# Optimization experiments

Measured on AMD Instinct MI355X. Metric: run time of the kernel, lower is better.

The kernel has to match this reference:

```python
import jax, jax.numpy as jnp
import numpy as np

B, C, H, W = 2, 512, 128, 128
L_NUM, HEADS, LEVELS, POINTS = 6, 8, 1, 4
HEAD_DIM = C // HEADS


def setup_inputs() -> dict:
    key = jax.random.key(0)
    ks = jax.random.split(key, 16)
    s = 0.02
    rn = lambda k, shape, scale=s: jax.random.normal(k, shape, jnp.float32) * scale
    return dict(
        bev_feat=jax.random.normal(ks[0], (B, C, H, W), jnp.float32),
        lidar_feat=jax.random.normal(ks[1], (B, C, H, W), jnp.float32),
        Wv=rn(ks[2], (L_NUM, C, C)), bv=jnp.zeros((L_NUM, C), jnp.float32),
        Woff=rn(ks[3], (L_NUM, C, HEADS * LEVELS * POINTS * 2)),
        boff=rn(ks[4], (L_NUM, HEADS * LEVELS * POINTS * 2), 0.5),
        Waw=rn(ks[5], (L_NUM, C, HEADS * LEVELS * POINTS)),
        baw=jnp.zeros((L_NUM, HEADS * LEVELS * POINTS), jnp.float32),
        Wout=rn(ks[6], (L_NUM, C, C)), bout=jnp.zeros((L_NUM, C), jnp.float32),
        ln1_g=jnp.ones((L_NUM, C), jnp.float32), ln1_b=jnp.zeros((L_NUM, C), jnp.float32),
        W1=rn(ks[7], (L_NUM, C, C)), W2=rn(ks[8], (L_NUM, C, C)),
        ln2_g=jnp.ones((L_NUM, C), jnp.float32), ln2_b=jnp.zeros((L_NUM, C), jnp.float32),
        pe_W1=rn(ks[9], (2, C), 0.5),
        pe_bn_g=jnp.ones((C,), jnp.float32), pe_bn_b=jnp.zeros((C,), jnp.float32),
        pe_bn_m=jnp.zeros((C,), jnp.float32), pe_bn_v=jnp.ones((C,), jnp.float32),
        pe_W2=rn(ks[10], (C, C)),
    )


def _layer_norm(x, g, b):
    mu = jnp.mean(x, -1, keepdims=True)
    var = jnp.mean((x - mu) ** 2, -1, keepdims=True)
    return (x - mu) * jax.lax.rsqrt(var + 1e-5) * g + b


def _bilinear_gather(v_flat, locx, locy):
    # v_flat: (B, heads, H*W, d); locx/locy: (B, heads, S) normalized [0,1]
    # grid_sample semantics: align_corners=False, zero padding
    x = locx * W - 0.5
    y = locy * H - 0.5
    x0f = jnp.floor(x); y0f = jnp.floor(y)
    wx = x - x0f; wy = y - y0f
    x0 = x0f.astype(jnp.int32); y0 = y0f.astype(jnp.int32)

    def corner(xi, yi, w):
        inb = (xi >= 0) & (xi < W) & (yi >= 0) & (yi < H)
        idx = jnp.clip(yi, 0, H - 1) * W + jnp.clip(xi, 0, W - 1)
        g = jnp.take_along_axis(v_flat, idx[..., None], axis=2)
        return g * (w * inb)[..., None]

    return (corner(x0, y0, (1 - wx) * (1 - wy)) + corner(x0 + 1, y0, wx * (1 - wy))
            + corner(x0, y0 + 1, (1 - wx) * wy) + corner(x0 + 1, y0 + 1, wx * wy))


def reference(bev_feat, lidar_feat, Wv, bv, Woff, boff, Waw, baw, Wout, bout,
              ln1_g, ln1_b, W1, W2, ln2_g, ln2_b,
              pe_W1, pe_bn_g, pe_bn_b, pe_bn_m, pe_bn_v, pe_W2):
    N = H * W
    # sparse voxelization: keep rows with all-nonzero features, pack valid-first per batch
    lf = jnp.transpose(lidar_feat, (0, 2, 3, 1)).reshape(B, N, C)
    mask = jnp.all(lf != 0, axis=-1)                       # (B,N)
    order = jnp.argsort((~mask).astype(jnp.int32), axis=1, stable=True)  # valid first
    valid = jnp.take_along_axis(mask, order, axis=1)       # (B,N)
    q = jnp.take_along_axis(lf, order[..., None], axis=1) * valid[..., None]
    hh = jnp.arange(N) // W
    ww = jnp.arange(N) % W
    ref_all = jnp.stack([ww / W, hh / H], -1).astype(jnp.float32)  # (N,2) = (x,y)
    ref = jnp.broadcast_to(ref_all, (B, N, 2))
    ref = jnp.take_along_axis(ref, order[..., None], axis=1) * valid[..., None]
    # learned positional embedding (BatchNorm in eval mode)
    pe = ref.reshape(B * N, 2) @ pe_W1
    pe = (pe - pe_bn_m) * jax.lax.rsqrt(pe_bn_v + 1e-5) * pe_bn_g + pe_bn_b
    q_pos = (jax.nn.relu(pe) @ pe_W2).reshape(B, N, C)
    feat_flat = jnp.transpose(bev_feat.reshape(B, C, N), (0, 2, 1))  # (B,N,C)
    norm_xy = jnp.array([W, H], jnp.float32)  # offset normalizer per level (w,h)
    for i in range(L_NUM):
        ident = q
        x = q + q_pos
        v = (feat_flat @ Wv[i] + bv[i]).reshape(B, N, HEADS, HEAD_DIM)
        v_flat = jnp.transpose(v, (0, 2, 1, 3))  # (B,heads,N,d)
        off = (x @ Woff[i] + boff[i]).reshape(B, N, HEADS, LEVELS * POINTS, 2)
        aw = jax.nn.softmax((x @ Waw[i] + baw[i]).reshape(B, N, HEADS, LEVELS * POINTS), axis=-1)
        loc = ref[:, :, None, None, :] + off / norm_xy      # (B,N,heads,P,2)
        locx = jnp.transpose(loc[..., 0], (0, 2, 1, 3)).reshape(B, HEADS, N * POINTS)
        locy = jnp.transpose(loc[..., 1], (0, 2, 1, 3)).reshape(B, HEADS, N * POINTS)
        samp = _bilinear_gather(v_flat, locx, locy).reshape(B, HEADS, N, POINTS, HEAD_DIM)
        awt = jnp.transpose(aw, (0, 2, 1, 3))               # (B,heads,N,P)
        out = jnp.sum(samp * awt[..., None], axis=3)        # (B,heads,N,d)
        out = jnp.transpose(out, (0, 2, 1, 3)).reshape(B, N, C)
        q = out @ Wout[i] + bout[i] + ident                 # dropout in eval = identity
        q = _layer_norm(q, ln1_g[i], ln1_b[i])
        q = jax.nn.relu(q @ W1[i]) @ W2[i] + q
        q = _layer_norm(q, ln2_g[i], ln2_b[i])
    # scatter back to dense (B,C,H,W); invalid voxels stay zero
    slots = jnp.zeros((B, N, C), q.dtype)
    slots = slots.at[jnp.arange(B)[:, None], order].set(q * valid[..., None])
    return jnp.transpose(slots.reshape(B, H, W, C), (0, 3, 1, 2))
```

## Files before the change

kernel.cpp:

```cpp
#include <hip/hip_runtime.h>
#include <cstdint>
#include <cstddef>

#define BDIM 2
#define CDIM 512
#define HDIM 128
#define WDIM 128
#define NDIM (HDIM * WDIM)
#define LNUM 6
#define NHEADS 8
#define HEAD_DIM 64
#define NPTS 4
#define BN_TOT (BDIM * NDIM)

typedef unsigned short u16;
typedef __attribute__((ext_vector_type(8))) short bf16x8;
typedef __attribute__((ext_vector_type(4))) float f32x4;

__device__ __forceinline__ u16 f2bf(float x) {
    unsigned u = __float_as_uint(x);
    u += 0x7fffu + ((u >> 16) & 1u);
    return (u16)(u >> 16);
}
__device__ __forceinline__ float bf2f(u16 h) {
    return __uint_as_float(((unsigned)h) << 16);
}

__device__ __forceinline__ void load_lds16(const void* g, void* l) {
    __builtin_amdgcn_global_load_lds(
        (const __attribute__((address_space(1))) void*)g,
        (__attribute__((address_space(3))) void*)l, 16, 0, 0);
}

__device__ __forceinline__ void wait_vm8() { asm volatile("s_waitcnt vmcnt(8)" ::: "memory"); }
__device__ __forceinline__ void wait_vm0() { asm volatile("s_waitcnt vmcnt(0)" ::: "memory"); }

__global__ void mask_kernel(const float* __restrict__ lidar, int* __restrict__ mask)
{
    int idx = blockIdx.x * blockDim.x + threadIdx.x;
    if (idx >= BN_TOT) return;
    int b = idx / NDIM;
    int n = idx - b * NDIM;
    const float* p = lidar + (size_t)b * CDIM * NDIM + n;
    int ok = 1;
#pragma unroll 8
    for (int c = 0; c < CDIM; ++c)
        ok &= (p[(size_t)c * NDIM] != 0.0f);
    mask[idx] = ok;
}

__global__ void order_kernel(const int* __restrict__ mask, int* __restrict__ order,
                             int* __restrict__ nvalid)
{
    int b = blockIdx.x;
    const int* m = mask + b * NDIM;
    int* ord = order + b * NDIM;
    __shared__ int part[256];
    __shared__ int totalValid;
    int t = threadIdx.x;
    const int CHUNK = NDIM / 256;
    int base = t * CHUNK;
    int cnt = 0;
    for (int i = 0; i < CHUNK; ++i) cnt += m[base + i];
    part[t] = cnt;
    __syncthreads();
    for (int s = 1; s < 256; s <<= 1) {
        int v = (t >= s) ? part[t - s] : 0;
        __syncthreads();
        part[t] += v;
        __syncthreads();
    }
    if (t == 255) { totalValid = part[255]; nvalid[b] = part[255]; }
    __syncthreads();
    int validBefore = (t == 0) ? 0 : part[t - 1];
    int nv = totalValid;
    for (int i = 0; i < CHUNK; ++i) {
        int n = base + i;
        if (m[n]) { ord[validBefore] = n; validBefore++; }
        else      { int invBefore = n - validBefore; ord[nv + invBefore] = n; }
    }
}

__global__ void ref_kernel(const int* __restrict__ order, const int* __restrict__ nvalid,
                           float* __restrict__ ref)
{
    int idx = blockIdx.x * blockDim.x + threadIdx.x;
    if (idx >= BN_TOT) return;
    int b = idx / NDIM;
    int j = idx - b * NDIM;
    int n = order[idx];
    float flag = (j < nvalid[b]) ? 1.0f : 0.0f;
    int hh = n / WDIM;
    int ww = n - hh * WDIM;
    ref[(size_t)idx * 2 + 0] = ((float)ww / (float)WDIM) * flag;
    ref[(size_t)idx * 2 + 1] = ((float)hh / (float)HDIM) * flag;
}

__global__ void pack_q_kernel(const float* __restrict__ lidar, const int* __restrict__ order,
                              const int* __restrict__ nvalid, u16* __restrict__ q)
{
    __shared__ float tile[32][33];
    __shared__ int ord_s[32];
    int b  = blockIdx.z;
    int j0 = blockIdx.x * 32;
    int c0 = blockIdx.y * 32;
    int tx = threadIdx.x, ty = threadIdx.y;
    if (ty == 0) ord_s[tx] = order[b * NDIM + j0 + tx];
    __syncthreads();
    const float* src = lidar + (size_t)b * CDIM * NDIM;
#pragma unroll
    for (int k = 0; k < 4; ++k) {
        int cl = ty * 4 + k;
        tile[cl][tx] = src[(size_t)(c0 + cl) * NDIM + ord_s[tx]];
    }
    __syncthreads();
    int nv = nvalid[b];
#pragma unroll
    for (int k = 0; k < 4; ++k) {
        int jl = ty * 4 + k;
        int j = j0 + jl;
        float f = (j < nv) ? 1.0f : 0.0f;
        q[((size_t)b * NDIM + j) * CDIM + c0 + tx] = f2bf(tile[tx][jl] * f);
    }
}

__global__ void scatter_kernel(const u16* __restrict__ q, const int* __restrict__ order,
                               const int* __restrict__ nvalid, float* __restrict__ out)
{
    __shared__ float tile[32][33];
    __shared__ int ord_s[32];
    int b  = blockIdx.z;
    int j0 = blockIdx.x * 32;
    int c0 = blockIdx.y * 32;
    int tx = threadIdx.x, ty = threadIdx.y;
    if (ty == 0) ord_s[tx] = order[b * NDIM + j0 + tx];
    __syncthreads();
    int nv = nvalid[b];
#pragma unroll
    for (int k = 0; k < 4; ++k) {
        int jl = ty * 4 + k;
        int j = j0 + jl;
        float f = (j < nv) ? 1.0f : 0.0f;
        tile[jl][tx] = bf2f(q[((size_t)b * NDIM + j) * CDIM + c0 + tx]) * f;
    }
    __syncthreads();
    float* dst = out + (size_t)b * CDIM * NDIM;
#pragma unroll
    for (int k = 0; k < 4; ++k) {
        int cl = ty * 4 + k;
        dst[(size_t)(c0 + cl) * NDIM + ord_s[tx]] = tile[tx][cl];
    }
}

__global__ void tconv_b_kernel(const float* __restrict__ src0, u16* __restrict__ dst0)
{
    __shared__ float t[32][33];
    int z = blockIdx.z;
    const float* src = src0 + (size_t)z * 512 * 512;
    u16* dst = dst0 + (size_t)z * 512 * 512;
    int k0 = blockIdx.x * 32, n0 = blockIdx.y * 32;
    int tx = threadIdx.x, ty = threadIdx.y;
#pragma unroll
    for (int j = 0; j < 4; ++j) {
        int kl = ty * 4 + j;
        t[kl][tx] = src[(size_t)(k0 + kl) * 512 + n0 + tx];
    }
    __syncthreads();
#pragma unroll
    for (int j = 0; j < 4; ++j) {
        int nl = ty * 4 + j;
        dst[(size_t)(n0 + nl) * 512 + k0 + tx] = f2bf(t[tx][nl]);
    }
}

__global__ void tconv_offaw_b_kernel(const float* __restrict__ woff0,
                                     const float* __restrict__ waw0,
                                     u16* __restrict__ dst0)
{
    __shared__ float t[32][33];
    int z = blockIdx.z;
    const float* woff = woff0 + (size_t)z * 512 * 64;
    const float* waw  = waw0 + (size_t)z * 512 * 32;
    u16* dst = dst0 + (size_t)z * 96 * 512;
    int k0 = blockIdx.x * 32, n0 = blockIdx.y * 32;
    int tx = threadIdx.x, ty = threadIdx.y;
#pragma unroll
    for (int j = 0; j < 4; ++j) {
        int kl = ty * 4 + j;
        int n = n0 + tx;
        float v = (n < 64) ? woff[(size_t)(k0 + kl) * 64 + n]
                           : waw[(size_t)(k0 + kl) * 32 + (n - 64)];
        t[kl][tx] = v;
    }
    __syncthreads();
#pragma unroll
    for (int j = 0; j < 4; ++j) {
        int nl = ty * 4 + j;
        dst[(size_t)(n0 + nl) * 512 + k0 + tx] = f2bf(t[tx][nl]);
    }
}

__global__ void bev_conv_kernel(const float* __restrict__ bev, u16* __restrict__ dst)
{
    __shared__ float t[32][33];
    int b  = blockIdx.z;
    int n0 = blockIdx.x * 32;
    int c0 = blockIdx.y * 32;
    int tx = threadIdx.x, ty = threadIdx.y;
    const float* src = bev + (size_t)b * CDIM * NDIM;
#pragma unroll
    for (int j = 0; j < 4; ++j) {
        int cl = ty * 4 + j;
        t[cl][tx] = src[(size_t)(c0 + cl) * NDIM + n0 + tx];
    }
    __syncthreads();
#pragma unroll
    for (int j = 0; j < 4; ++j) {
        int nl = ty * 4 + j;
        dst[((size_t)b * NDIM + n0 + nl) * CDIM + c0 + tx] = f2bf(t[tx][nl]);
    }
}

__global__ void pe_hidden_kernel(const float* __restrict__ ref, const float* __restrict__ W1,
                                 const float* __restrict__ g, const float* __restrict__ bb,
                                 const float* __restrict__ m, const float* __restrict__ v,
                                 u16* __restrict__ out)
{
    int row = blockIdx.x;
    float r0 = ref[(size_t)row * 2 + 0];
    float r1 = ref[(size_t)row * 2 + 1];
    for (int c = threadIdx.x; c < CDIM; c += blockDim.x) {
        float pe = r0 * W1[c] + r1 * W1[CDIM + c];
        pe = (pe - m[c]) * rsqrtf(v[c] + 1e-5f) * g[c] + bb[c];
        out[(size_t)row * CDIM + c] = f2bf(fmaxf(pe, 0.0f));
    }
}

__global__ void add_bf_kernel(const u16* __restrict__ q, const u16* __restrict__ qpos,
                              u16* __restrict__ x)
{
    size_t i = (size_t)blockIdx.x * blockDim.x + threadIdx.x;
    uint4 qa = ((const uint4*)q)[i];
    uint4 pv = ((const uint4*)qpos)[i];
    unsigned qw[4] = {qa.x, qa.y, qa.z, qa.w};
    unsigned pw[4] = {pv.x, pv.y, pv.z, pv.w};
    unsigned rw[4];
#pragma unroll
    for (int k = 0; k < 4; ++k) {
        float a0 = bf2f((u16)(qw[k] & 0xffff)), a1 = bf2f((u16)(qw[k] >> 16));
        float p0 = bf2f((u16)(pw[k] & 0xffff)), p1 = bf2f((u16)(pw[k] >> 16));
        rw[k] = (unsigned)f2bf(a0 + p0) | ((unsigned)f2bf(a1 + p1) << 16);
    }
    uint4 r; r.x = rw[0]; r.y = rw[1]; r.z = rw[2]; r.w = rw[3];
    ((uint4*)x)[i] = r;
}

__global__ __launch_bounds__(256) void gemm_bf16(
    const u16* __restrict__ A, const u16* __restrict__ Bt,
    const float* __restrict__ bias, u16* __restrict__ outB, int relu)
{
    __shared__ u16 As[2][128 * 32];
    __shared__ u16 Bs[2][128 * 32];
    int tid = threadIdx.x;
    int wave = tid >> 6, lane = tid & 63;
    int wr = wave >> 1, wc = wave & 1;
    int quad = lane >> 4, l15 = lane & 15;
    int bm = blockIdx.y * 128, bn = blockIdx.x * 128;

    f32x4 acc[4][4];
#pragma unroll
    for (int i = 0; i < 4; ++i)
#pragma unroll
        for (int j = 0; j < 4; ++j) { f32x4 z = {0.f, 0.f, 0.f, 0.f}; acc[i][j] = z; }

    const u16* Ag[4];
    const u16* Bg[4];
#pragma unroll
    for (int s = 0; s < 4; ++s) {
        Ag[s] = A  + (size_t)(bm + wr * 64 + s * 16 + (lane >> 2)) * 512 + (lane & 3) * 8;
        Bg[s] = Bt + (size_t)(bn + wc * 64 + s * 16 + (lane >> 2)) * 512 + (lane & 3) * 8;
    }

#pragma unroll
    for (int s = 0; s < 4; ++s) {
        load_lds16(Ag[s], &As[0][(wr * 4 + s) * 512]);
        load_lds16(Bg[s], &Bs[0][(wc * 4 + s) * 512]);
    }

    for (int it = 0; it < 16; ++it) {
        __builtin_amdgcn_s_barrier();
        int cur = it & 1, nxt = cur ^ 1;
        if (it < 15) {
            int kn = (it + 1) * 32;
#pragma unroll
            for (int s = 0; s < 4; ++s) {
                load_lds16(Ag[s] + kn, &As[nxt][(wr * 4 + s) * 512]);
                load_lds16(Bg[s] + kn, &Bs[nxt][(wc * 4 + s) * 512]);
            }
            wait_vm8();
        } else {
            wait_vm0();
        }
        bf16x8 av[4], bv[4];
#pragma unroll
        for (int mi = 0; mi < 4; ++mi)
            av[mi] = *(const bf16x8*)&As[cur][(wr * 64 + mi * 16 + l15) * 32 + quad * 8];
#pragma unroll
        for (int ni = 0; ni < 4; ++ni)
            bv[ni] = *(const bf16x8*)&Bs[cur][(wc * 64 + ni * 16 + l15) * 32 + quad * 8];
#pragma unroll
        for (int mi = 0; mi < 4; ++mi)
#pragma unroll
            for (int ni = 0; ni < 4; ++ni)
                acc[mi][ni] = __builtin_amdgcn_mfma_f32_16x16x32_bf16(
                    av[mi], bv[ni], acc[mi][ni], 0, 0, 0);
    }

    int rowb = bm + wr * 64;
    int colb = bn + wc * 64;
#pragma unroll
    for (int mi = 0; mi < 4; ++mi) {
#pragma unroll
        for (int ni = 0; ni < 4; ++ni) {
            int col = colb + ni * 16 + l15;
            float bi = bias ? bias[col] : 0.0f;
#pragma unroll
            for (int r = 0; r < 4; ++r) {
                int row = rowb + mi * 16 + quad * 4 + r;
                float val = acc[mi][ni][r] + bi;
                if (relu) val = fmaxf(val, 0.0f);
                outB[(size_t)row * 512 + col] = f2bf(val);
            }
        }
    }
}

__global__ __launch_bounds__(512, 4) void gemm_ln(
    const u16* __restrict__ A, const u16* __restrict__ Bt,
    const float* __restrict__ bias, const u16* __restrict__ resid,
    const float* __restrict__ g, const float* __restrict__ bta,
    u16* __restrict__ outQ, const u16* __restrict__ qpos, u16* __restrict__ outX)
{
    __shared__ u16 As[2][64 * 32];
    __shared__ u16 Bs[2][512 * 32];
    __shared__ float rs[8][64];
    __shared__ float rq[8][64];
    __shared__ float muL[64], invL[64];

    int tid = threadIdx.x;
    int wv = tid >> 6, lane = tid & 63;
    int quad = lane >> 4, l15 = lane & 15;
    int bm = blockIdx.x * 64;

    f32x4 acc[4][4];
#pragma unroll
    for (int i = 0; i < 4; ++i)
#pragma unroll
        for (int j = 0; j < 4; ++j) { f32x4 z = {0.f, 0.f, 0.f, 0.f}; acc[i][j] = z; }

    const u16* Ag[4];
    const u16* Bg[4];
#pragma unroll
    for (int s = 0; s < 4; ++s) {
        Ag[s] = A  + (size_t)(bm + s * 16 + (lane >> 2)) * 512 + (lane & 3) * 8;
        Bg[s] = Bt + (size_t)((wv * 4 + s) * 16 + (lane >> 2)) * 512 + (lane & 3) * 8;
    }

#pragma unroll
    for (int s = 0; s < 4; ++s) {
        load_lds16(Ag[s], &As[0][s * 512]);
        load_lds16(Bg[s], &Bs[0][(wv * 4 + s) * 512]);
    }

    for (int kk = 0; kk < 16; ++kk) {
        __builtin_amdgcn_s_barrier();
        int cur = kk & 1, nxt = cur ^ 1;
        if (kk < 15) {
            int kn = (kk + 1) * 32;
#pragma unroll
            for (int s = 0; s < 4; ++s) {
                load_lds16(Ag[s] + kn, &As[nxt][s * 512]);
                load_lds16(Bg[s] + kn, &Bs[nxt][(wv * 4 + s) * 512]);
            }
            wait_vm8();
        } else {
            wait_vm0();
        }
        bf16x8 av[4], bv[4];
#pragma unroll
        for (int mi = 0; mi < 4; ++mi)
            av[mi] = *(const bf16x8*)&As[cur][(mi * 16 + l15) * 32 + quad * 8];
#pragma unroll
        for (int ni = 0; ni < 4; ++ni)
            bv[ni] = *(const bf16x8*)&Bs[cur][(wv * 64 + ni * 16 + l15) * 32 + quad * 8];
#pragma unroll
        for (int mi = 0; mi < 4; ++mi)
#pragma unroll
            for (int ni = 0; ni < 4; ++ni)
                acc[mi][ni] = __builtin_amdgcn_mfma_f32_16x16x32_bf16(
                    av[mi], bv[ni], acc[mi][ni], 0, 0, 0);
    }

    int colb = wv * 64;
    float biasv[4], gv[4], btv[4];
#pragma unroll
    for (int ni = 0; ni < 4; ++ni) {
        int c = colb + ni * 16 + l15;
        biasv[ni] = bias ? bias[c] : 0.0f;
        gv[ni] = g[c];
        btv[ni] = bta[c];
    }
#pragma unroll
    for (int mi = 0; mi < 4; ++mi) {
#pragma unroll
        for (int r = 0; r < 4; ++r) {
            size_t rowoff = (size_t)(bm + mi * 16 + quad * 4 + r) * 512;
#pragma unroll
            for (int ni = 0; ni < 4; ++ni) {
                int col = colb + ni * 16 + l15;
                acc[mi][ni][r] += biasv[ni] + bf2f(resid[rowoff + col]);
            }
        }
    }
#pragma unroll
    for (int mi = 0; mi < 4; ++mi) {
#pragma unroll
        for (int r = 0; r < 4; ++r) {
            float s = acc[mi][0][r] + acc[mi][1][r] + acc[mi][2][r] + acc[mi][3][r];
            float s2 = acc[mi][0][r] * acc[mi][0][r] + acc[mi][1][r] * acc[mi][1][r]
                     + acc[mi][2][r] * acc[mi][2][r] + acc[mi][3][r] * acc[mi][3][r];
#pragma unroll
            for (int m = 1; m < 16; m <<= 1) {
                s  += __shfl_xor(s, m, 64);
                s2 += __shfl_xor(s2, m, 64);
            }
            if (l15 == 0) {
                rs[wv][mi * 16 + quad * 4 + r] = s;
                rq[wv][mi * 16 + quad * 4 + r] = s2;
            }
        }
    }
    __syncthreads();
    if (tid < 64) {
        float s = 0.f, s2 = 0.f;
#pragma unroll
        for (int w = 0; w < 8; ++w) { s += rs[w][tid]; s2 += rq[w][tid]; }
        float mu = s * (1.0f / 512.0f);
        float var = s2 * (1.0f / 512.0f) - mu * mu;
        muL[tid] = mu;
        invL[tid] = rsqrtf(var + 1e-5f);
    }
    __syncthreads();
#pragma unroll
    for (int mi = 0; mi < 4; ++mi) {
#pragma unroll
        for (int r = 0; r < 4; ++r) {
            int lrow = mi * 16 + quad * 4 + r;
            float mu = muL[lrow], iv = invL[lrow];
            size_t rowoff = (size_t)(bm + lrow) * 512;
#pragma unroll
            for (int ni = 0; ni < 4; ++ni) {
                int col = colb + ni * 16 + l15;
                float y = (acc[mi][ni][r] - mu) * iv * gv[ni] + btv[ni];
                outQ[rowoff + col] = f2bf(y);
                if (outX)
                    outX[rowoff + col] = f2bf(y + bf2f(qpos[rowoff + col]));
            }
        }
    }
}

__global__ __launch_bounds__(256) void gemm_offaw(
    const u16* __restrict__ A, const u16* __restrict__ Bt,
    const float* __restrict__ boff, const float* __restrict__ baw,
    u16* __restrict__ offb, u16* __restrict__ awb)
{
    __shared__ u16 As[2][128 * 32];
    __shared__ u16 Bs[2][128 * 32];
    int tid = threadIdx.x;
    int wave = tid >> 6, lane = tid & 63;
    int wr = wave >> 1, wc = wave & 1;
    int quad = lane >> 4, l15 = lane & 15;
    int bm = blockIdx.y * 128;

    f32x4 acc[4][4];
#pragma unroll
    for (int i = 0; i < 4; ++i)
#pragma unroll
        for (int j = 0; j < 4; ++j) { f32x4 z = {0.f, 0.f, 0.f, 0.f}; acc[i][j] = z; }

    const u16* Ag[4];
    const u16* Bg[4];
#pragma unroll
    for (int s = 0; s < 4; ++s) {
        Ag[s] = A + (size_t)(bm + wr * 64 + s * 16 + (lane >> 2)) * 512 + (lane & 3) * 8;
        int br = wc * 64 + s * 16 + (lane >> 2);
        if (br > 95) br = 95;
        Bg[s] = Bt + (size_t)br * 512 + (lane & 3) * 8;
    }

#pragma unroll
    for (int s = 0; s < 4; ++s) {
        load_lds16(Ag[s], &As[0][(wr * 4 + s) * 512]);
        load_lds16(Bg[s], &Bs[0][(wc * 4 + s) * 512]);
    }

    for (int it = 0; it < 16; ++it) {
        __builtin_amdgcn_s_barrier();
        int cur = it & 1, nxt = cur ^ 1;
        if (it < 15) {
            int kn = (it + 1) * 32;
#pragma unroll
            for (int s = 0; s < 4; ++s) {
                load_lds16(Ag[s] + kn, &As[nxt][(wr * 4 + s) * 512]);
                load_lds16(Bg[s] + kn, &Bs[nxt][(wc * 4 + s) * 512]);
            }
            wait_vm8();
        } else {
            wait_vm0();
        }
        bf16x8 av[4], bv[4];
#pragma unroll
        for (int mi = 0; mi < 4; ++mi)
            av[mi] = *(const bf16x8*)&As[cur][(wr * 64 + mi * 16 + l15) * 32 + quad * 8];
#pragma unroll
        for (int ni = 0; ni < 4; ++ni)
            bv[ni] = *(const bf16x8*)&Bs[cur][(wc * 64 + ni * 16 + l15) * 32 + quad * 8];
#pragma unroll
        for (int mi = 0; mi < 4; ++mi)
#pragma unroll
            for (int ni = 0; ni < 4; ++ni)
                acc[mi][ni] = __builtin_amdgcn_mfma_f32_16x16x32_bf16(
                    av[mi], bv[ni], acc[mi][ni], 0, 0, 0);
    }

    int rowb = bm + wr * 64;
#pragma unroll
    for (int mi = 0; mi < 4; ++mi) {
#pragma unroll
        for (int ni = 0; ni < 4; ++ni) {
            int col = wc * 64 + ni * 16 + l15;
            if (col < 96) {
                float bi = (col < 64) ? boff[col] : baw[col - 64];
#pragma unroll
                for (int r = 0; r < 4; ++r) {
                    int row = rowb + mi * 16 + quad * 4 + r;
                    float val = acc[mi][ni][r] + bi;
                    if (col < 64) offb[(size_t)row * 64 + col] = f2bf(val);
                    else          awb[(size_t)row * 32 + (col - 64)] = f2bf(val);
                }
            }
        }
    }
}

__global__ __launch_bounds__(256) void sample_kernel(
    const float* __restrict__ ref, const u16* __restrict__ off,
    const u16* __restrict__ aw, const u16* __restrict__ v,
    u16* __restrict__ out)
{
    int bj = blockIdx.x * 4 + (threadIdx.x >> 6);
    int lane = threadIdx.x & 63;
    int h  = lane >> 3;
    int d8 = (lane & 7) * 8;
    int b  = bj >> 14;

    float rx = ref[(size_t)bj * 2 + 0];
    float ry = ref[(size_t)bj * 2 + 1];
    uint4 offv = *(const uint4*)(off + (size_t)bj * 64 + h * 8);
    uint2 awv  = *(const uint2*)(aw + (size_t)bj * 32 + h * 4);

    float l0 = bf2f((u16)(awv.x & 0xffff)), l1 = bf2f((u16)(awv.x >> 16));
    float l2 = bf2f((u16)(awv.y & 0xffff)), l3 = bf2f((u16)(awv.y >> 16));
    float mx = fmaxf(fmaxf(l0, l1), fmaxf(l2, l3));
    float e[4];
    e[0] = expf(l0 - mx); e[1] = expf(l1 - mx);
    e[2] = expf(l2 - mx); e[3] = expf(l3 - mx);
    float inv_es = 1.0f / (e[0] + e[1] + e[2] + e[3]);

    const u16* vb = v + (size_t)b * NDIM * CDIM + h * HEAD_DIM + d8;
    float acc[8] = {0.f, 0.f, 0.f, 0.f, 0.f, 0.f, 0.f, 0.f};
    unsigned ow[4] = {offv.x, offv.y, offv.z, offv.w};

#pragma unroll
    for (int p = 0; p < NPTS; ++p) {
        float ox = bf2f((u16)(ow[p] & 0xffff));
        float oy = bf2f((u16)(ow[p] >> 16));
        float X = rx * (float)WDIM + ox - 0.5f;
        float Y = ry * (float)HDIM + oy - 0.5f;
        float x0f = floorf(X), y0f = floorf(Y);
        float wx = X - x0f, wy = Y - y0f;
        int x0 = (int)x0f, y0 = (int)y0f;
        float ep = e[p];
#pragma unroll
        for (int cy = 0; cy < 2; ++cy) {
            int yy = y0 + cy;
            float wyc = cy ? wy : (1.0f - wy);
            int yin = (yy >= 0) & (yy < HDIM);
            int yc = min(max(yy, 0), HDIM - 1);
#pragma unroll
            for (int cx = 0; cx < 2; ++cx) {
                int xx = x0 + cx;
                float wxc = cx ? wx : (1.0f - wx);
                int xin = (xx >= 0) & (xx < WDIM);
                int xc = min(max(xx, 0), WDIM - 1);
                float wgt = ep * wyc * wxc * (float)(yin & xin);
                uint4 vv = *(const uint4*)(vb + (size_t)(yc * WDIM + xc) * CDIM);
                acc[0] += wgt * bf2f((u16)(vv.x & 0xffff));
                acc[1] += wgt * bf2f((u16)(vv.x >> 16));
                acc[2] += wgt * bf2f((u16)(vv.y & 0xffff));
                acc[3] += wgt * bf2f((u16)(vv.y >> 16));
                acc[4] += wgt * bf2f((u16)(vv.z & 0xffff));
                acc[5] += wgt * bf2f((u16)(vv.z >> 16));
                acc[6] += wgt * bf2f((u16)(vv.w & 0xffff));
                acc[7] += wgt * bf2f((u16)(vv.w >> 16));
            }
        }
    }
    uint4 r;
    r.x = (unsigned)f2bf(acc[0] * inv_es) | ((unsigned)f2bf(acc[1] * inv_es) << 16);
    r.y = (unsigned)f2bf(acc[2] * inv_es) | ((unsigned)f2bf(acc[3] * inv_es) << 16);
    r.z = (unsigned)f2bf(acc[4] * inv_es) | ((unsigned)f2bf(acc[5] * inv_es) << 16);
    r.w = (unsigned)f2bf(acc[6] * inv_es) | ((unsigned)f2bf(acc[7] * inv_es) << 16);
    *(uint4*)(out + (size_t)bj * CDIM + h * HEAD_DIM + d8) = r;
}

extern "C" void kernel_launch(void* const* d_in, const int* in_sizes, int n_in,
                              void* d_out, int out_size, void* d_ws, size_t ws_size,
                              hipStream_t stream)
{
    const float* bev   = (const float*)d_in[0];
    const float* lidar = (const float*)d_in[1];
    const float* Wv    = (const float*)d_in[2];
    const float* bv    = (const float*)d_in[3];
    const float* Woff  = (const float*)d_in[4];
    const float* boff  = (const float*)d_in[5];
    const float* Waw   = (const float*)d_in[6];
    const float* baw   = (const float*)d_in[7];
    const float* Wout  = (const float*)d_in[8];
    const float* bout  = (const float*)d_in[9];
    const float* ln1g  = (const float*)d_in[10];
    const float* ln1b  = (const float*)d_in[11];
    const float* W1    = (const float*)d_in[12];
    const float* W2    = (const float*)d_in[13];
    const float* ln2g  = (const float*)d_in[14];
    const float* ln2b  = (const float*)d_in[15];
    const float* peW1  = (const float*)d_in[16];
    const float* peg   = (const float*)d_in[17];
    const float* peb   = (const float*)d_in[18];
    const float* pem   = (const float*)d_in[19];
    const float* pev   = (const float*)d_in[20];
    const float* peW2  = (const float*)d_in[21];

    const size_t NC = (size_t)BN_TOT * CDIM;
    const size_t WSZ = 512 * 512;

    char* base = (char*)d_ws;
    u16* q      = (u16*)base;
    u16* actA   = (u16*)(base + NC * 2);
    u16* actB   = (u16*)(base + NC * 4);
    u16* wt     = (u16*)(base + NC * 6);
    u16* wtv    = wt;
    u16* wtout  = wt + 6 * WSZ;
    u16* wt1    = wt + 12 * WSZ;
    u16* wt2    = wt + 18 * WSZ;
    u16* wtpe   = wt + 24 * WSZ;
    u16* offawt = wt + 25 * WSZ;
    u16* offb   = offawt + 6 * 96 * 512;
    u16* awb    = offb + (size_t)BN_TOT * 64;
    float* refb = (float*)(awb + (size_t)BN_TOT * 32);
    int* mask   = (int*)(refb + (size_t)BN_TOT * 2);
    int* order  = mask + BN_TOT;
    int* nvalid = order + BN_TOT;

    u16* qpos_bf = (u16*)d_out;
    u16* featT   = (u16*)d_out + NC;

    dim3 blk328(32, 8);
    dim3 gemm_grid(4, 256);
    dim3 offaw_grid(1, 256);
    int  ln_grid = BN_TOT / 64;

    mask_kernel<<<BN_TOT / 256, 256, 0, stream>>>(lidar, mask);
    order_kernel<<<BDIM, 256, 0, stream>>>(mask, order, nvalid);
    ref_kernel<<<BN_TOT / 256, 256, 0, stream>>>(order, nvalid, refb);
    pack_q_kernel<<<dim3(NDIM / 32, CDIM / 32, BDIM), blk328, 0, stream>>>(lidar, order, nvalid, q);
    bev_conv_kernel<<<dim3(NDIM / 32, CDIM / 32, BDIM), blk328, 0, stream>>>(bev, featT);

    tconv_b_kernel<<<dim3(16, 16, 6), blk328, 0, stream>>>(Wv,   wtv);
    tconv_b_kernel<<<dim3(16, 16, 6), blk328, 0, stream>>>(Wout, wtout);
    tconv_b_kernel<<<dim3(16, 16, 6), blk328, 0, stream>>>(W1,   wt1);
    tconv_b_kernel<<<dim3(16, 16, 6), blk328, 0, stream>>>(W2,   wt2);
    tconv_b_kernel<<<dim3(16, 16, 1), blk328, 0, stream>>>(peW2, wtpe);
    tconv_offaw_b_kernel<<<dim3(16, 3, 6), blk328, 0, stream>>>(Woff, Waw, offawt);

    pe_hidden_kernel<<<BN_TOT, 128, 0, stream>>>(refb, peW1, peg, peb, pem, pev, actA);
    gemm_bf16<<<gemm_grid, 256, 0, stream>>>(actA, wtpe, nullptr, qpos_bf, 0);

    add_bf_kernel<<<(unsigned)(NC / 8 / 256), 256, 0, stream>>>(q, qpos_bf, actB);

    for (int i = 0; i < LNUM; ++i) {
        gemm_offaw<<<offaw_grid, 256, 0, stream>>>(actB, offawt + (size_t)i * 96 * 512,
                                                   boff + i * 64, baw + i * 32, offb, awb);
        gemm_bf16<<<gemm_grid, 256, 0, stream>>>(featT, wtv + (size_t)i * WSZ,
                                                 bv + i * CDIM, actA, 0);
        sample_kernel<<<BN_TOT / 4, 256, 0, stream>>>(refb, offb, awb, actA, actB);
        gemm_ln<<<ln_grid, 512, 0, stream>>>(actB, wtout + (size_t)i * WSZ, bout + i * CDIM,
                                             q, ln1g + i * CDIM, ln1b + i * CDIM,
                                             q, nullptr, nullptr);
        gemm_bf16<<<gemm_grid, 256, 0, stream>>>(q, wt1 + (size_t)i * WSZ, nullptr, actA, 1);
        gemm_ln<<<ln_grid, 512, 0, stream>>>(actA, wt2 + (size_t)i * WSZ, nullptr,
                                             q, ln2g + i * CDIM, ln2b + i * CDIM,
                                             q, qpos_bf,
                                             (i < LNUM - 1) ? actB : nullptr);
    }

    scatter_kernel<<<dim3(NDIM / 32, CDIM / 32, BDIM), blk328, 0, stream>>>(
        q, order, nvalid, (float*)d_out);
}
```

Measured before the change: 1.864 ms.

## Enlarge gemm_ln row tile, spread tile loads across waves, add post-load barriers

gemm_ln now computes 128 rows per block instead of 64, with a 2x4 wave grid where each wave holds a 64x128 accumulator tile. This halves how often the full 512-column weight tile is reloaded per row and halves the grid size. gemm_bf16 now splits its A/B tile loads cooperatively across waves (two chunks each) and adds a second barrier after the vmcnt wait so the LDS data from other waves is visible; gemm_ln does the same. The costs are more accumulator registers in gemm_ln (128 floats, with the occupancy hint of 4 dropped), half as many blocks, and an extra barrier per k-step.

Result: no change. 1.875 ms (+0.6%).

```diff
diff --git a/kernel.cpp b/kernel.cpp
--- a/kernel.cpp
+++ b/kernel.cpp
@@ -33,7 +33,11 @@
 }
 
 __device__ __forceinline__ void wait_vm8() { asm volatile("s_waitcnt vmcnt(8)" ::: "memory"); }
+__device__ __forceinline__ void wait_vm5() { asm volatile("s_waitcnt vmcnt(5)" ::: "memory"); }
+__device__ __forceinline__ void wait_vm4() { asm volatile("s_waitcnt vmcnt(4)" ::: "memory"); }
 __device__ __forceinline__ void wait_vm0() { asm volatile("s_waitcnt vmcnt(0)" ::: "memory"); }
+__device__ __forceinline__ void sbar()  { __builtin_amdgcn_s_barrier(); }
+__device__ __forceinline__ void spin()  { __builtin_amdgcn_sched_barrier(0); }
 
 __global__ void mask_kernel(const float* __restrict__ lidar, int* __restrict__ mask)
 {
@@ -273,34 +277,31 @@
 #pragma unroll
         for (int j = 0; j < 4; ++j) { f32x4 z = {0.f, 0.f, 0.f, 0.f}; acc[i][j] = z; }
 
-    const u16* Ag[4];
-    const u16* Bg[4];
-#pragma unroll
-    for (int s = 0; s < 4; ++s) {
-        Ag[s] = A  + (size_t)(bm + wr * 64 + s * 16 + (lane >> 2)) * 512 + (lane & 3) * 8;
-        Bg[s] = Bt + (size_t)(bn + wc * 64 + s * 16 + (lane >> 2)) * 512 + (lane & 3) * 8;
-    }
-
-#pragma unroll
-    for (int s = 0; s < 4; ++s) {
-        load_lds16(Ag[s], &As[0][(wr * 4 + s) * 512]);
-        load_lds16(Bg[s], &Bs[0][(wc * 4 + s) * 512]);
-    }
+    int ch0 = wave, ch1 = wave + 4;
+    const u16* Ag0 = A  + (size_t)(bm + ch0 * 16 + (lane >> 2)) * 512 + (lane & 3) * 8;
+    const u16* Ag1 = A  + (size_t)(bm + ch1 * 16 + (lane >> 2)) * 512 + (lane & 3) * 8;
+    const u16* Bg0 = Bt + (size_t)(bn + ch0 * 16 + (lane >> 2)) * 512 + (lane & 3) * 8;
+    const u16* Bg1 = Bt + (size_t)(bn + ch1 * 16 + (lane >> 2)) * 512 + (lane & 3) * 8;
+
+    load_lds16(Ag0, &As[0][ch0 * 512]);
+    load_lds16(Ag1, &As[0][ch1 * 512]);
+    load_lds16(Bg0, &Bs[0][ch0 * 512]);
+    load_lds16(Bg1, &Bs[0][ch1 * 512]);
 
     for (int it = 0; it < 16; ++it) {
-        __builtin_amdgcn_s_barrier();
+        sbar();  spin();
         int cur = it & 1, nxt = cur ^ 1;
         if (it < 15) {
             int kn = (it + 1) * 32;
-#pragma unroll
-            for (int s = 0; s < 4; ++s) {
-                load_lds16(Ag[s] + kn, &As[nxt][(wr * 4 + s) * 512]);
-                load_lds16(Bg[s] + kn, &Bs[nxt][(wc * 4 + s) * 512]);
-            }
-            wait_vm8();
+            load_lds16(Ag0 + kn, &As[nxt][ch0 * 512]);
+            load_lds16(Ag1 + kn, &As[nxt][ch1 * 512]);
+            load_lds16(Bg0 + kn, &Bs[nxt][ch0 * 512]);
+            load_lds16(Bg1 + kn, &Bs[nxt][ch1 * 512]);
+            wait_vm4();
         } else {
             wait_vm0();
         }
+        sbar();  spin();
         bf16x8 av[4], bv[4];
 #pragma unroll
         for (int mi = 0; mi < 4; ++mi)
@@ -335,76 +336,74 @@
     }
 }
 
-__global__ __launch_bounds__(512, 4) void gemm_ln(
+__global__ __launch_bounds__(512) void gemm_ln(
     const u16* __restrict__ A, const u16* __restrict__ Bt,
     const float* __restrict__ bias, const u16* __restrict__ resid,
     const float* __restrict__ g, const float* __restrict__ bta,
     u16* __restrict__ outQ, const u16* __restrict__ qpos, u16* __restrict__ outX)
 {
-    __shared__ u16 As[2][64 * 32];
+    __shared__ u16 As[2][128 * 32];
     __shared__ u16 Bs[2][512 * 32];
     __shared__ float rs[8][64];
     __shared__ float rq[8][64];
-    __shared__ float muL[64], invL[64];
+    __shared__ float muL[128], invL[128];
 
     int tid = threadIdx.x;
     int wv = tid >> 6, lane = tid & 63;
     int quad = lane >> 4, l15 = lane & 15;
-    int bm = blockIdx.x * 64;
-
-    f32x4 acc[4][4];
+    int wr = wv >> 2, wc = wv & 3;
+    int bm = blockIdx.x * 128;
+
+    f32x4 acc[4][8];
 #pragma unroll
     for (int i = 0; i < 4; ++i)
 #pragma unroll
-        for (int j = 0; j < 4; ++j) { f32x4 z = {0.f, 0.f, 0.f, 0.f}; acc[i][j] = z; }
-
-    const u16* Ag[4];
+        for (int j = 0; j < 8; ++j) { f32x4 z = {0.f, 0.f, 0.f, 0.f}; acc[i][j] = z; }
+
+    const u16* Ag = A + (size_t)(bm + wv * 16 + (lane >> 2)) * 512 + (lane & 3) * 8;
     const u16* Bg[4];
 #pragma unroll
-    for (int s = 0; s < 4; ++s) {
-        Ag[s] = A  + (size_t)(bm + s * 16 + (lane >> 2)) * 512 + (lane & 3) * 8;
+    for (int s = 0; s < 4; ++s)
         Bg[s] = Bt + (size_t)((wv * 4 + s) * 16 + (lane >> 2)) * 512 + (lane & 3) * 8;
-    }
-
-#pragma unroll
-    for (int s = 0; s < 4; ++s) {
-        load_lds16(Ag[s], &As[0][s * 512]);
+
+    load_lds16(Ag, &As[0][wv * 512]);
+#pragma unroll
+    for (int s = 0; s < 4; ++s)
         load_lds16(Bg[s], &Bs[0][(wv * 4 + s) * 512]);
-    }
 
     for (int kk = 0; kk < 16; ++kk) {
-        __builtin_amdgcn_s_barrier();
+        sbar();  spin();
         int cur = kk & 1, nxt = cur ^ 1;
         if (kk < 15) {
             int kn = (kk + 1) * 32;
-#pragma unroll
-            for (int s = 0; s < 4; ++s) {
-                load_lds16(Ag[s] + kn, &As[nxt][s * 512]);
+            load_lds16(Ag + kn, &As[nxt][wv * 512]);
+#pragma unroll
+            for (int s = 0; s < 4; ++s)
                 load_lds16(Bg[s] + kn, &Bs[nxt][(wv * 4 + s) * 512]);
-            }
-            wait_vm8();
+            wait_vm5();
         } else {
             wait_vm0();
         }
-        bf16x8 av[4], bv[4];
+        sbar();  spin();
+        bf16x8 av[4], bv[8];
 #pragma unroll
         for (int mi = 0; mi < 4; ++mi)
-            av[mi] = *(const bf16x8*)&As[cur][(mi * 16 + l15) * 32 + quad * 8];
-#pragma unroll
-        for (int ni = 0; ni < 4; ++ni)
-            bv[ni] = *(const bf16x8*)&Bs[cur][(wv * 64 + ni * 16 + l15) * 32 + quad * 8];
+            av[mi] = *(const bf16x8*)&As[cur][(wr * 64 + mi * 16 + l15) * 32 + quad * 8];
+#pragma unroll
+        for (int ni = 0; ni < 8; ++ni)
+            bv[ni] = *(const bf16x8*)&Bs[cur][(wc * 128 + ni * 16 + l15) * 32 + quad * 8];
 #pragma unroll
         for (int mi = 0; mi < 4; ++mi)
 #pragma unroll
-            for (int ni = 0; ni < 4; ++ni)
+            for (int ni = 0; ni < 8; ++ni)
                 acc[mi][ni] = __builtin_amdgcn_mfma_f32_16x16x32_bf16(
                     av[mi], bv[ni], acc[mi][ni], 0, 0, 0);
     }
 
-    int colb = wv * 64;
-    float biasv[4], gv[4], btv[4];
-#pragma unroll
-    for (int ni = 0; ni < 4; ++ni) {
+    int colb = wc * 128;
+    float biasv[8], gv[8], btv[8];
+#pragma unroll
+    for (int ni = 0; ni < 8; ++ni) {
         int c = colb + ni * 16 + l15;
         biasv[ni] = bias ? bias[c] : 0.0f;
         gv[ni] = g[c];
@@ -414,9 +413,9 @@
     for (int mi = 0; mi < 4; ++mi) {
 #pragma unroll
         for (int r = 0; r < 4; ++r) {
-            size_t rowoff = (size_t)(bm + mi * 16 + quad * 4 + r) * 512;
-#pragma unroll
-            for (int ni = 0; ni < 4; ++ni) {
+            size_t rowoff = (size_t)(bm + wr * 64 + mi * 16 + quad * 4 + r) * 512;
+#pragma unroll
+            for (int ni = 0; ni < 8; ++ni) {
                 int col = colb + ni * 16 + l15;
                 acc[mi][ni][r] += biasv[ni] + bf2f(resid[rowoff + col]);
             }
@@ -426,9 +425,12 @@
     for (int mi = 0; mi < 4; ++mi) {
 #pragma unroll
         for (int r = 0; r < 4; ++r) {
-            float s = acc[mi][0][r] + acc[mi][1][r] + acc[mi][2][r] + acc[mi][3][r];
-            float s2 = acc[mi][0][r] * acc[mi][0][r] + acc[mi][1][r] * acc[mi][1][r]
-                     + acc[mi][2][r] * acc[mi][2][r] + acc[mi][3][r] * acc[mi][3][r];
+            float s = 0.f, s2 = 0.f;
+#pragma unroll
+            for (int ni = 0; ni < 8; ++ni) {
+                s  += acc[mi][ni][r];
+                s2 += acc[mi][ni][r] * acc[mi][ni][r];
+            }
 #pragma unroll
             for (int m = 1; m < 16; m <<= 1) {
                 s  += __shfl_xor(s, m, 64);
@@ -441,10 +443,14 @@
         }
     }
     __syncthreads();
-    if (tid < 64) {
+    if (tid < 128) {
+        int wrg = tid >> 6, lr = tid & 63;
         float s = 0.f, s2 = 0.f;
 #pragma unroll
-        for (int w = 0; w < 8; ++w) { s += rs[w][tid]; s2 += rq[w][tid]; }
+        for (int w4 = 0; w4 < 4; ++w4) {
+            int w = wrg * 4 + w4;
+            s += rs[w][lr]; s2 += rq[w][lr];
+        }
         float mu = s * (1.0f / 512.0f);
         float var = s2 * (1.0f / 512.0f) - mu * mu;
         muL[tid] = mu;
@@ -455,11 +461,11 @@
     for (int mi = 0; mi < 4; ++mi) {
 #pragma unroll
         for (int r = 0; r < 4; ++r) {
-            int lrow = mi * 16 + quad * 4 + r;
+            int lrow = wr * 64 + mi * 16 + quad * 4 + r;
             float mu = muL[lrow], iv = invL[lrow];
             size_t rowoff = (size_t)(bm + lrow) * 512;
 #pragma unroll
-            for (int ni = 0; ni < 4; ++ni) {
+            for (int ni = 0; ni < 8; ++ni) {
                 int col = colb + ni * 16 + l15;
                 float y = (acc[mi][ni][r] - mu) * iv * gv[ni] + btv[ni];
                 outQ[rowoff + col] = f2bf(y);
@@ -506,7 +512,7 @@
     }
 
     for (int it = 0; it < 16; ++it) {
-        __builtin_amdgcn_s_barrier();
+        sbar();
         int cur = it & 1, nxt = cur ^ 1;
         if (it < 15) {
             int kn = (it + 1) * 32;
@@ -679,7 +685,7 @@
     dim3 blk328(32, 8);
     dim3 gemm_grid(4, 256);
     dim3 offaw_grid(1, 256);
-    int  ln_grid = BN_TOT / 64;
+    int  ln_grid = BN_TOT / 128;
 
     mask_kernel<<<BN_TOT / 256, 256, 0, stream>>>(lidar, mask);
     order_kernel<<<BDIM, 256, 0, stream>>>(mask, order, nvalid);
```
